# Kernel tuning notes

Measured on AMD Instinct MI355X. Metric: run time of the kernel, lower is better.

Reference implementation:

```python
import jax, jax.numpy as jnp
import numpy as np

B, F, D = 4096, 39, 16
L0, L1 = 128, 128
H1 = L0 // 2  # split_half: half the maps feed the next layer


def setup_inputs() -> dict:
    key = jax.random.key(0)
    k0, k1, k2, k3, k4 = jax.random.split(key, 5)
    x = jax.random.normal(k0, (B, F, D), dtype=jnp.float32)
    # Conv1D(size, 1, channels_first) == matmul over channel dim: W [out, in]
    W0 = jax.random.normal(k1, (L0, F * F), dtype=jnp.float32) * 0.02
    b0 = jnp.zeros((L0,), dtype=jnp.float32)
    W1 = jax.random.normal(k2, (L1, H1 * F), dtype=jnp.float32) * 0.02
    b1 = jnp.zeros((L1,), dtype=jnp.float32)
    return {"x": x, "W0": W0, "b0": b0, "W1": W1, "b1": b1}


def _cin_layer(h, h0, W, b):
    # h: [B, H, D], h0: [B, F, D] -> outer product [B, H*F, D], then 1x1 conv
    z = jnp.einsum('bhd,bmd->bhmd', h, h0)
    z = z.reshape(z.shape[0], -1, z.shape[-1])          # [B, H*F, D]
    y = jnp.einsum('oc,bcd->bod', W, z) + b[None, :, None]
    return jax.nn.relu(y)


def reference(x, W0, b0, W1, b1):
    h0 = x
    # layer 0 (split_half, not last): split into next_hidden / direct_connect
    y0 = _cin_layer(h0, h0, W0, b0)                     # [B, L0, D]
    next_hidden, direct0 = y0[:, :H1, :], y0[:, H1:, :]
    # layer 1 (last): all maps are direct connect
    direct1 = _cin_layer(next_hidden, h0, W1, b1)       # [B, L1, D]
    result = jnp.sum(jnp.concatenate([direct0, direct1], axis=1), axis=-1)
    return result  # [B, L0//2 + L1]
```

## Files before the change

kernel.cpp:

```cpp
#include <hip/hip_runtime.h>
#include <hip/hip_fp16.h>

#define B_    4096
#define F_    39
#define D_    16
#define L0_   128
#define H1_   64
#define NKK0  50
#define NKK1  80
#define NKK   (NKK0+NKK1)
#define WP_ELEMS (NKK*8*64*8)

typedef _Float16 f16x8 __attribute__((ext_vector_type(8)));
typedef float    f32x4 __attribute__((ext_vector_type(4)));

union Frag {
    f16x8   h8;
    __half2 h2[4];
    f32x4   f4v;
};

__device__ __forceinline__ void gload_lds16(const void* g, void* l) {
    __builtin_amdgcn_global_load_lds(
        (const __attribute__((address_space(1))) void*)g,
        (__attribute__((address_space(3))) void*)l, 16, 0, 0);
}

__global__ __launch_bounds__(256) void prep_w(
    const float* __restrict__ W0, const float* __restrict__ W1,
    __half* __restrict__ Wp)
{
    int idx = blockIdx.x * 256 + threadIdx.x;
    if (idx >= WP_ELEMS) return;
    int j    = idx & 7;
    int l    = (idx >> 3) & 63;
    int tile = (idx >> 9) & 7;
    int kk   = idx >> 12;
    int lg = l >> 4;
    int o  = tile * 16 + (l & 15);
    float v = 0.f;
    if (kk < NKK0) {
        int u = kk * 4 + lg;
        int h = u / 5, a = u - 5 * (u / 5);
        int m = a * 8 + j;
        if (h < F_ && m < F_) v = W0[o * (F_ * F_) + h * F_ + m];
    } else {
        int u = (kk - NKK0) * 4 + lg;
        int h = u / 5, a = u - 5 * (u / 5);
        int m = a * 8 + j;
        if (m < F_) v = W1[o * (H1_ * F_) + h * F_ + m];
    }
    Wp[idx] = __float2half(v);
}

__global__ __launch_bounds__(256, 2) void cin_main(
    const float* __restrict__ x, const float* __restrict__ b0,
    const float* __restrict__ b1, const __half* __restrict__ Wp,
    float* __restrict__ out)
{
    __shared__ __align__(16) __half Wl[2][2][8][64][8];
    __shared__ __align__(16) __half xT [8][16][40];
    __shared__ __align__(16) __half nhT[8][16][68];

    const int t    = threadIdx.x;
    const int w    = t >> 6;
    const int lane = t & 63;
    const int d    = lane & 15;
    const int lg   = lane >> 4;
    const int gbase = blockIdx.x * 8 + w * 2;

#pragma unroll
    for (int bt = 0; bt < 2; ++bt) {
        const float* xb = x + (size_t)(gbase + bt) * (F_ * D_);
        const int wbt = w * 2 + bt;
        for (int i = lane; i < 640; i += 64) {
            float xv = (i < F_ * D_) ? xb[i] : 0.f;
            xT[wbt][i & 15][i >> 4] = __float2half(xv);
        }
    }

    f32x4 acc[8][2];
#pragma unroll
    for (int tt = 0; tt < 8; ++tt) {
        f32x4 bb = *(const f32x4*)&b0[tt * 16 + lg * 4];
        acc[tt][0] = bb; acc[tt][1] = bb;
    }

    auto stage = [&](int r, int buf) {
        const __half* src = Wp + (size_t)r * 8192;
#pragma unroll
        for (int it = 0; it < 4; ++it) {
            gload_lds16(src + it * 2048 + t * 8,
                        &Wl[buf][0][0][0][0] + it * 2048 + t * 8);
        }
    };

    int buf = 0;
    stage(0, 0);
    asm volatile("s_waitcnt vmcnt(0)" ::: "memory");
    __syncthreads();

    for (int r = 0; r < NKK / 2; ++r) {
        if (r < NKK / 2 - 1) stage(r + 1, buf ^ 1);

#pragma unroll
        for (int kk2 = 0; kk2 < 2; ++kk2) {
            const int kk = 2 * r + kk2;

            if (kk == NKK0) {
#pragma unroll
                for (int tt = 0; tt < 8; ++tt) {
#pragma unroll
                    for (int bt = 0; bt < 2; ++bt) {
                        float v0 = fmaxf(acc[tt][bt][0], 0.f);
                        float v1 = fmaxf(acc[tt][bt][1], 0.f);
                        float v2 = fmaxf(acc[tt][bt][2], 0.f);
                        float v3 = fmaxf(acc[tt][bt][3], 0.f);
                        const int wbt = w * 2 + bt;
                        if (tt < 4) {
                            const int o = tt * 16 + lg * 4;
                            *(__half2*)&nhT[wbt][d][o]     = __floats2half2_rn(v0, v1);
                            *(__half2*)&nhT[wbt][d][o + 2] = __floats2half2_rn(v2, v3);
                        } else {
#pragma unroll
                            for (int msk = 1; msk <= 8; msk <<= 1) {
                                v0 += __shfl_xor(v0, msk, 64);
                                v1 += __shfl_xor(v1, msk, 64);
                                v2 += __shfl_xor(v2, msk, 64);
                                v3 += __shfl_xor(v3, msk, 64);
                            }
                            if (d == 0) {
                                float4 s; s.x = v0; s.y = v1; s.z = v2; s.w = v3;
                                *(float4*)&out[(size_t)(gbase + bt) * 192 +
                                               tt * 16 + lg * 4 - 64] = s;
                            }
                        }
                    }
                }
#pragma unroll
                for (int tt = 0; tt < 8; ++tt) {
                    f32x4 bb = *(const f32x4*)&b1[tt * 16 + lg * 4];
                    acc[tt][0] = bb; acc[tt][1] = bb;
                }
            }

            const int  kl = (kk < NKK0) ? kk : kk - NKK0;
            const int  u  = kl * 4 + lg;
            const int  h  = (u * 52429) >> 18;
            const int  a  = u - 5 * h;
            const bool L0 = (kk < NKK0);

            Frag bfr[2];
#pragma unroll
            for (int bt = 0; bt < 2; ++bt) {
                const int wbt = w * 2 + bt;
                const __half* xhrow = L0 ? &xT[wbt][d][0] : &nhT[wbt][d][0];
                __half2 xh2 = __half2half2(xhrow[h]);
                Frag xm;
                xm.f4v = *(const f32x4*)&xT[wbt][d][a * 8];
#pragma unroll
                for (int q = 0; q < 4; ++q)
                    bfr[bt].h2[q] = __hmul2(xm.h2[q], xh2);
            }

#pragma unroll
            for (int tt = 0; tt < 8; ++tt) {
                Frag af;
                af.f4v = *(const f32x4*)&Wl[buf][kk2][tt][lane][0];
#pragma unroll
                for (int bt = 0; bt < 2; ++bt)
                    acc[tt][bt] = __builtin_amdgcn_mfma_f32_16x16x32_f16(
                        af.h8, bfr[bt].h8, acc[tt][bt], 0, 0, 0);
            }
        }
        asm volatile("s_waitcnt vmcnt(0)" ::: "memory");
        __syncthreads();
        buf ^= 1;
    }

#pragma unroll
    for (int tt = 0; tt < 8; ++tt) {
#pragma unroll
        for (int bt = 0; bt < 2; ++bt) {
            float v0 = fmaxf(acc[tt][bt][0], 0.f);
            float v1 = fmaxf(acc[tt][bt][1], 0.f);
            float v2 = fmaxf(acc[tt][bt][2], 0.f);
            float v3 = fmaxf(acc[tt][bt][3], 0.f);
#pragma unroll
            for (int msk = 1; msk <= 8; msk <<= 1) {
                v0 += __shfl_xor(v0, msk, 64);
                v1 += __shfl_xor(v1, msk, 64);
                v2 += __shfl_xor(v2, msk, 64);
                v3 += __shfl_xor(v3, msk, 64);
            }
            if (d == 0) {
                float4 s; s.x = v0; s.y = v1; s.z = v2; s.w = v3;
                *(float4*)&out[(size_t)(gbase + bt) * 192 + 64 + tt * 16 + lg * 4] = s;
            }
        }
    }
}

extern "C" void kernel_launch(void* const* d_in, const int* in_sizes, int n_in,
                              void* d_out, int out_size, void* d_ws, size_t ws_size,
                              hipStream_t stream) {
    const float* x  = (const float*)d_in[0];
    const float* W0 = (const float*)d_in[1];
    const float* b0 = (const float*)d_in[2];
    const float* W1 = (const float*)d_in[3];
    const float* b1 = (const float*)d_in[4];
    float* out = (float*)d_out;
    __half* Wp = (__half*)d_ws;

    prep_w<<<(WP_ELEMS + 255) / 256, 256, 0, stream>>>(W0, W1, Wp);
    cin_main<<<B_ / 8, 256, 0, stream>>>(x, b0, b1, Wp, out);
}
```

Baseline: 85.98 us.

## Switch CIN kernel to 32x32x16 MFMA with register-cached x fragments

Replaces the 16x16x32 MFMA tiling with 32x32x16 MFMAs. Each wave pair now splits the output rows, and each wave covers four batch samples packed into the N dimension. The K ordering is changed so the x-fragment chunk index stays constant across a group of rounds, letting the fragments sit in registers instead of being reloaded from LDS. The x load is vectorized to float4. The aim is fewer LDS reads and MFMA instructions per unit of work, at the cost of more complex indexing, higher register pressure, and scalar output stores.

```diff
diff --git a/kernel.cpp b/kernel.cpp
--- a/kernel.cpp
+++ b/kernel.cpp
@@ -4,21 +4,17 @@
 #define B_    4096
 #define F_    39
 #define D_    16
-#define L0_   128
-#define H1_   64
 #define NKK0  50
 #define NKK1  80
-#define NKK   (NKK0+NKK1)
-#define WP_ELEMS (NKK*8*64*8)
-
-typedef _Float16 f16x8 __attribute__((ext_vector_type(8)));
-typedef float    f32x4 __attribute__((ext_vector_type(4)));
-
-union Frag {
-    f16x8   h8;
-    __half2 h2[4];
-    f32x4   f4v;
-};
+#define NKK   130
+#define NRND  65
+#define WP_HALFS (NKK * 4096)
+
+typedef _Float16 f16x8  __attribute__((ext_vector_type(8)));
+typedef float    f32x4  __attribute__((ext_vector_type(4)));
+typedef float    f32x16 __attribute__((ext_vector_type(16)));
+
+union FragAB { f16x8 h8; __half2 h2[4]; f32x4 f4; __half h[8]; };
 
 __device__ __forceinline__ void gload_lds16(const void* g, void* l) {
     __builtin_amdgcn_global_load_lds(
@@ -31,26 +27,74 @@
     __half* __restrict__ Wp)
 {
     int idx = blockIdx.x * 256 + threadIdx.x;
-    if (idx >= WP_ELEMS) return;
-    int j    = idx & 7;
-    int l    = (idx >> 3) & 63;
-    int tile = (idx >> 9) & 7;
-    int kk   = idx >> 12;
-    int lg = l >> 4;
-    int o  = tile * 16 + (l & 15);
+    if (idx >= WP_HALFS) return;
+    int j   = idx & 7;
+    int l   = (idx >> 3) & 63;
+    int ks  = (idx >> 9) & 1;
+    int Mt  = (idx >> 10) & 3;
+    int kkg = idx >> 12;
+    int o   = Mt * 32 + (l & 31);
+    int sub = l >> 5;
     float v = 0.f;
-    if (kk < NKK0) {
-        int u = kk * 4 + lg;
-        int h = u / 5, a = u - 5 * (u / 5);
-        int m = a * 8 + j;
+    if (kkg < NKK0) {
+        int u = 4 * kkg + 2 * ks + sub;
+        int a = u / 40, h = u - 40 * a, m = a * 8 + j;
         if (h < F_ && m < F_) v = W0[o * (F_ * F_) + h * F_ + m];
     } else {
-        int u = (kk - NKK0) * 4 + lg;
-        int h = u / 5, a = u - 5 * (u / 5);
-        int m = a * 8 + j;
-        if (m < F_) v = W1[o * (H1_ * F_) + h * F_ + m];
+        int u = 4 * (kkg - NKK0) + 2 * ks + sub;
+        int a = u >> 6, h = u & 63, m = a * 8 + j;
+        if (m < F_) v = W1[o * (64 * F_) + h * F_ + m];
     }
     Wp[idx] = __float2half(v);
+}
+
+template<int LL, int AA>
+__device__ __forceinline__ void do_round(
+    int rr, int t, int sub,
+    const __half* xrowA, const __half* xrowB,
+    const __half* nrowA, const __half* nrowB,
+    const FragAB (&xmc)[2][5], f32x16 (&acc)[2][2],
+    __half* WlFlat, int wl_thread,
+    int& buf, int& rg, const __half*& wsrc)
+{
+    if (rg < NRND - 1) {
+        __half* dst = WlFlat + (buf ^ 1) * 8192;
+#pragma unroll
+        for (int it = 0; it < 4; ++it)
+            gload_lds16(wsrc + it * 2048 + t * 8, dst + it * 2048 + t * 8);
+        wsrc += 8192;
+    }
+    const __half* wl  = WlFlat + buf * 8192 + wl_thread;
+    const __half* hbA = LL ? nrowA : xrowA;
+    const __half* hbB = LL ? nrowB : xrowB;
+
+#pragma unroll
+    for (int kk2 = 0; kk2 < 2; ++kk2) {
+#pragma unroll
+        for (int ks = 0; ks < 2; ++ks) {
+            const int hoff = 8 * rr + 4 * kk2 + 2 * ks + sub;
+            __half2 xa2 = __half2half2(hbA[hoff]);
+            __half2 xb2 = __half2half2(hbB[hoff]);
+            FragAB bA, bB;
+#pragma unroll
+            for (int q = 0; q < 4; ++q) {
+                bA.h2[q] = __hmul2(xmc[0][AA].h2[q], xa2);
+                bB.h2[q] = __hmul2(xmc[1][AA].h2[q], xb2);
+            }
+#pragma unroll
+            for (int mt = 0; mt < 2; ++mt) {
+                FragAB A;
+                A.f4 = *(const f32x4*)(wl + kk2 * 4096 + mt * 1024 + ks * 512);
+                acc[mt][0] = __builtin_amdgcn_mfma_f32_32x32x16_f16(
+                    A.h8, bA.h8, acc[mt][0], 0, 0, 0);
+                acc[mt][1] = __builtin_amdgcn_mfma_f32_32x32x16_f16(
+                    A.h8, bB.h8, acc[mt][1], 0, 0, 0);
+            }
+        }
+    }
+    asm volatile("s_waitcnt vmcnt(0)" ::: "memory");
+    __syncthreads();
+    buf ^= 1; ++rg;
 }
 
 __global__ __launch_bounds__(256, 2) void cin_main(
@@ -58,144 +102,148 @@
     const float* __restrict__ b1, const __half* __restrict__ Wp,
     float* __restrict__ out)
 {
-    __shared__ __align__(16) __half Wl[2][2][8][64][8];
-    __shared__ __align__(16) __half xT [8][16][40];
+    __shared__ __align__(16) __half Wl[2][8192];
+    __shared__ __align__(16) __half xT[8][16][40];
     __shared__ __align__(16) __half nhT[8][16][68];
 
     const int t    = threadIdx.x;
-    const int w    = t >> 6;
-    const int lane = t & 63;
-    const int d    = lane & 15;
-    const int lg   = lane >> 4;
-    const int gbase = blockIdx.x * 8 + w * 2;
-
-#pragma unroll
-    for (int bt = 0; bt < 2; ++bt) {
-        const float* xb = x + (size_t)(gbase + bt) * (F_ * D_);
-        const int wbt = w * 2 + bt;
-        for (int i = lane; i < 640; i += 64) {
-            float xv = (i < F_ * D_) ? xb[i] : 0.f;
-            xT[wbt][i & 15][i >> 4] = __float2half(xv);
-        }
-    }
-
-    f32x4 acc[8][2];
-#pragma unroll
-    for (int tt = 0; tt < 8; ++tt) {
-        f32x4 bb = *(const f32x4*)&b0[tt * 16 + lg * 4];
-        acc[tt][0] = bb; acc[tt][1] = bb;
-    }
-
-    auto stage = [&](int r, int buf) {
-        const __half* src = Wp + (size_t)r * 8192;
-#pragma unroll
-        for (int it = 0; it < 4; ++it) {
-            gload_lds16(src + it * 2048 + t * 8,
-                        &Wl[buf][0][0][0][0] + it * 2048 + t * 8);
-        }
-    };
-
-    int buf = 0;
-    stage(0, 0);
+    const int w    = t >> 6, lane = t & 63;
+    const int sub  = lane >> 5, bp = (lane >> 4) & 1, d = lane & 15;
+    const int g    = w >> 1, hi = w & 1;
+    const int gb   = blockIdx.x * 8;
+
+#pragma unroll
+    for (int it = 0; it < 4; ++it)
+        gload_lds16(Wp + it * 2048 + t * 8, &Wl[0][0] + it * 2048 + t * 8);
+
+    for (int i = t; i < 8 * 156; i += 256) {
+        int bt = i / 156, r2 = i - bt * 156;
+        int f = r2 >> 2, dq = r2 & 3;
+        const float4 v = *(const float4*)&x[((size_t)(gb + bt) * F_ + f) * D_ + dq * 4];
+        xT[bt][dq * 4 + 0][f] = __float2half(v.x);
+        xT[bt][dq * 4 + 1][f] = __float2half(v.y);
+        xT[bt][dq * 4 + 2][f] = __float2half(v.z);
+        xT[bt][dq * 4 + 3][f] = __float2half(v.w);
+    }
+    if (t < 128) xT[t >> 4][t & 15][39] = __float2half(0.f);
+
     asm volatile("s_waitcnt vmcnt(0)" ::: "memory");
     __syncthreads();
 
-    for (int r = 0; r < NKK / 2; ++r) {
-        if (r < NKK / 2 - 1) stage(r + 1, buf ^ 1);
-
-#pragma unroll
-        for (int kk2 = 0; kk2 < 2; ++kk2) {
-            const int kk = 2 * r + kk2;
-
-            if (kk == NKK0) {
-#pragma unroll
-                for (int tt = 0; tt < 8; ++tt) {
-#pragma unroll
-                    for (int bt = 0; bt < 2; ++bt) {
-                        float v0 = fmaxf(acc[tt][bt][0], 0.f);
-                        float v1 = fmaxf(acc[tt][bt][1], 0.f);
-                        float v2 = fmaxf(acc[tt][bt][2], 0.f);
-                        float v3 = fmaxf(acc[tt][bt][3], 0.f);
-                        const int wbt = w * 2 + bt;
-                        if (tt < 4) {
-                            const int o = tt * 16 + lg * 4;
-                            *(__half2*)&nhT[wbt][d][o]     = __floats2half2_rn(v0, v1);
-                            *(__half2*)&nhT[wbt][d][o + 2] = __floats2half2_rn(v2, v3);
-                        } else {
-#pragma unroll
-                            for (int msk = 1; msk <= 8; msk <<= 1) {
-                                v0 += __shfl_xor(v0, msk, 64);
-                                v1 += __shfl_xor(v1, msk, 64);
-                                v2 += __shfl_xor(v2, msk, 64);
-                                v3 += __shfl_xor(v3, msk, 64);
-                            }
-                            if (d == 0) {
-                                float4 s; s.x = v0; s.y = v1; s.z = v2; s.w = v3;
-                                *(float4*)&out[(size_t)(gbase + bt) * 192 +
-                                               tt * 16 + lg * 4 - 64] = s;
-                            }
-                        }
+    const int btA = g * 4 + bp;
+    const int btB = g * 4 + 2 + bp;
+    const __half* xrowA = &xT[btA][d][0];
+    const __half* xrowB = &xT[btB][d][0];
+    const __half* nrowA = &nhT[btA][d][0];
+    const __half* nrowB = &nhT[btB][d][0];
+    FragAB xmc[2][5];
+#pragma unroll
+    for (int a = 0; a < 5; ++a) {
+        xmc[0][a].f4 = *(const f32x4*)(xrowA + a * 8);
+        xmc[1][a].f4 = *(const f32x4*)(xrowB + a * 8);
+    }
+
+    f32x16 acc[2][2];
+#pragma unroll
+    for (int mt = 0; mt < 2; ++mt) {
+        const int Mt = hi * 2 + mt;
+#pragma unroll
+        for (int r = 0; r < 16; ++r) {
+            float bv = b0[Mt * 32 + (r & 3) + 8 * (r >> 2) + 4 * sub];
+            acc[mt][0][r] = bv; acc[mt][1][r] = bv;
+        }
+    }
+
+    const int wl_thread = (hi * 2) * 1024 + lane * 8;
+    __half* WlFlat = &Wl[0][0];
+    int buf = 0, rg = 0;
+    const __half* wsrc = Wp + 8192;
+
+#pragma unroll 1
+    for (int rr = 0; rr < 5; ++rr) do_round<0,0>(rr,t,sub,xrowA,xrowB,nrowA,nrowB,xmc,acc,WlFlat,wl_thread,buf,rg,wsrc);
+#pragma unroll 1
+    for (int rr = 0; rr < 5; ++rr) do_round<0,1>(rr,t,sub,xrowA,xrowB,nrowA,nrowB,xmc,acc,WlFlat,wl_thread,buf,rg,wsrc);
+#pragma unroll 1
+    for (int rr = 0; rr < 5; ++rr) do_round<0,2>(rr,t,sub,xrowA,xrowB,nrowA,nrowB,xmc,acc,WlFlat,wl_thread,buf,rg,wsrc);
+#pragma unroll 1
+    for (int rr = 0; rr < 5; ++rr) do_round<0,3>(rr,t,sub,xrowA,xrowB,nrowA,nrowB,xmc,acc,WlFlat,wl_thread,buf,rg,wsrc);
+#pragma unroll 1
+    for (int rr = 0; rr < 5; ++rr) do_round<0,4>(rr,t,sub,xrowA,xrowB,nrowA,nrowB,xmc,acc,WlFlat,wl_thread,buf,rg,wsrc);
+
+    if (hi) {
+#pragma unroll
+        for (int mt = 0; mt < 2; ++mt) {
+            const int Mt = 2 + mt;
+#pragma unroll
+            for (int p = 0; p < 2; ++p) {
+#pragma unroll
+                for (int r = 0; r < 16; ++r) {
+                    float v = fmaxf(acc[mt][p][r], 0.f);
+                    v += __shfl_xor(v, 1); v += __shfl_xor(v, 2);
+                    v += __shfl_xor(v, 4); v += __shfl_xor(v, 8);
+                    if (d == 0) {
+                        int row = Mt * 32 + (r & 3) + 8 * (r >> 2) + 4 * sub;
+                        int b   = gb + g * 4 + p * 2 + bp;
+                        out[(size_t)b * 192 + (row - 64)] = v;
                     }
                 }
-#pragma unroll
-                for (int tt = 0; tt < 8; ++tt) {
-                    f32x4 bb = *(const f32x4*)&b1[tt * 16 + lg * 4];
-                    acc[tt][0] = bb; acc[tt][1] = bb;
+            }
+        }
+    } else {
+#pragma unroll
+        for (int mt = 0; mt < 2; ++mt) {
+#pragma unroll
+            for (int p = 0; p < 2; ++p) {
+                __half* nr = (__half*)(p ? nrowB : nrowA);
+#pragma unroll
+                for (int rg4 = 0; rg4 < 4; ++rg4) {
+                    union { __half h[4]; float2 f2; } pk;
+#pragma unroll
+                    for (int q = 0; q < 4; ++q)
+                        pk.h[q] = __float2half(fmaxf(acc[mt][p][rg4 * 4 + q], 0.f));
+                    int row0 = mt * 32 + 8 * rg4 + 4 * sub;
+                    *(float2*)(nr + row0) = pk.f2;
                 }
             }
-
-            const int  kl = (kk < NKK0) ? kk : kk - NKK0;
-            const int  u  = kl * 4 + lg;
-            const int  h  = (u * 52429) >> 18;
-            const int  a  = u - 5 * h;
-            const bool L0 = (kk < NKK0);
-
-            Frag bfr[2];
-#pragma unroll
-            for (int bt = 0; bt < 2; ++bt) {
-                const int wbt = w * 2 + bt;
-                const __half* xhrow = L0 ? &xT[wbt][d][0] : &nhT[wbt][d][0];
-                __half2 xh2 = __half2half2(xhrow[h]);
-                Frag xm;
-                xm.f4v = *(const f32x4*)&xT[wbt][d][a * 8];
-#pragma unroll
-                for (int q = 0; q < 4; ++q)
-                    bfr[bt].h2[q] = __hmul2(xm.h2[q], xh2);
-            }
-
-#pragma unroll
-            for (int tt = 0; tt < 8; ++tt) {
-                Frag af;
-                af.f4v = *(const f32x4*)&Wl[buf][kk2][tt][lane][0];
-#pragma unroll
-                for (int bt = 0; bt < 2; ++bt)
-                    acc[tt][bt] = __builtin_amdgcn_mfma_f32_16x16x32_f16(
-                        af.h8, bfr[bt].h8, acc[tt][bt], 0, 0, 0);
-            }
-        }
-        asm volatile("s_waitcnt vmcnt(0)" ::: "memory");
-        __syncthreads();
-        buf ^= 1;
-    }
-
-#pragma unroll
-    for (int tt = 0; tt < 8; ++tt) {
-#pragma unroll
-        for (int bt = 0; bt < 2; ++bt) {
-            float v0 = fmaxf(acc[tt][bt][0], 0.f);
-            float v1 = fmaxf(acc[tt][bt][1], 0.f);
-            float v2 = fmaxf(acc[tt][bt][2], 0.f);
-            float v3 = fmaxf(acc[tt][bt][3], 0.f);
-#pragma unroll
-            for (int msk = 1; msk <= 8; msk <<= 1) {
-                v0 += __shfl_xor(v0, msk, 64);
-                v1 += __shfl_xor(v1, msk, 64);
-                v2 += __shfl_xor(v2, msk, 64);
-                v3 += __shfl_xor(v3, msk, 64);
-            }
-            if (d == 0) {
-                float4 s; s.x = v0; s.y = v1; s.z = v2; s.w = v3;
-                *(float4*)&out[(size_t)(gbase + bt) * 192 + 64 + tt * 16 + lg * 4] = s;
+        }
+    }
+#pragma unroll
+    for (int mt = 0; mt < 2; ++mt) {
+        const int Mt = hi * 2 + mt;
+#pragma unroll
+        for (int r = 0; r < 16; ++r) {
+            float bv = b1[Mt * 32 + (r & 3) + 8 * (r >> 2) + 4 * sub];
+            acc[mt][0][r] = bv; acc[mt][1][r] = bv;
+        }
+    }
+    __syncthreads();
+
+#pragma unroll 1
+    for (int rr = 0; rr < 8; ++rr) do_round<1,0>(rr,t,sub,xrowA,xrowB,nrowA,nrowB,xmc,acc,WlFlat,wl_thread,buf,rg,wsrc);
+#pragma unroll 1
+    for (int rr = 0; rr < 8; ++rr) do_round<1,1>(rr,t,sub,xrowA,xrowB,nrowA,nrowB,xmc,acc,WlFlat,wl_thread,buf,rg,wsrc);
+#pragma unroll 1
+    for (int rr = 0; rr < 8; ++rr) do_round<1,2>(rr,t,sub,xrowA,xrowB,nrowA,nrowB,xmc,acc,WlFlat,wl_thread,buf,rg,wsrc);
+#pragma unroll 1
+    for (int rr = 0; rr < 8; ++rr) do_round<1,3>(rr,t,sub,xrowA,xrowB,nrowA,nrowB,xmc,acc,WlFlat,wl_thread,buf,rg,wsrc);
+#pragma unroll 1
+    for (int rr = 0; rr < 8; ++rr) do_round<1,4>(rr,t,sub,xrowA,xrowB,nrowA,nrowB,xmc,acc,WlFlat,wl_thread,buf,rg,wsrc);
+
+#pragma unroll
+    for (int mt = 0; mt < 2; ++mt) {
+        const int Mt = hi * 2 + mt;
+#pragma unroll
+        for (int p = 0; p < 2; ++p) {
+#pragma unroll
+            for (int r = 0; r < 16; ++r) {
+                float v = fmaxf(acc[mt][p][r], 0.f);
+                v += __shfl_xor(v, 1); v += __shfl_xor(v, 2);
+                v += __shfl_xor(v, 4); v += __shfl_xor(v, 8);
+                if (d == 0) {
+                    int row = Mt * 32 + (r & 3) + 8 * (r >> 2) + 4 * sub;
+                    int b   = gb + g * 4 + p * 2 + bp;
+                    out[(size_t)b * 192 + 64 + row] = v;
+                }
             }
         }
     }
@@ -212,6 +260,6 @@
     float* out = (float*)d_out;
     __half* Wp = (__half*)d_ws;
 
-    prep_w<<<(WP_ELEMS + 255) / 256, 256, 0, stream>>>(W0, W1, Wp);
+    prep_w<<<(WP_HALFS + 255) / 256, 256, 0, stream>>>(W0, W1, Wp);
     cin_main<<<B_ / 8, 256, 0, stream>>>(x, b0, b1, Wp, out);
 }
```

New measurement: 87.89 us. 1.02x slower.
